# Optimization experiments

Hardware: AMD Instinct MI355X
Metric: run time of the kernel (lower is better)

Reference implementation:

```python
import jax, jax.numpy as jnp
import numpy as np

EPS_NORM = 1e-5   # RMSLayerNorm eps (hardcoded in __init__)
Q_EPS = 1e-5      # clamp floor for quantization scales (BitMat convention)


def _rmsnorm(x, w, eps):
    var = jnp.mean(jnp.square(x), axis=-1, keepdims=True)
    return x * jax.lax.rsqrt(var + eps) * w


def _weight_quant(w):
    # ternary (1.58-bit) quantization: scale = 1/mean(|W|), round+clip to {-1,0,1}
    scale = 1.0 / jnp.maximum(jnp.mean(jnp.abs(w)), Q_EPS)
    wq = jnp.clip(jnp.round(w * scale), -1.0, 1.0)
    return wq, scale


def _act_quant(x):
    # per-token int8 quantization: scale = 127/max(|x|) along last dim
    scale = 127.0 / jnp.maximum(jnp.max(jnp.abs(x), axis=-1, keepdims=True), Q_EPS)
    xq = jnp.clip(jnp.round(x * scale), -128.0, 127.0)
    return xq, scale


def setup_inputs() -> dict:
    key = jax.random.key(0)
    k1, k2 = jax.random.split(key)
    B, S, D = 4, 4096, 4096  # in_features == out_features == 4096
    x = jax.random.normal(k1, (B, S, D), dtype=jnp.float32)
    norm_weight = jnp.ones((D,), dtype=jnp.float32)
    # kaiming_normal fan_out relu: std = sqrt(2/out_features)
    weight = jax.random.normal(k2, (D, D), dtype=jnp.float32) * np.sqrt(2.0 / D)
    return {"x": x, "norm_weight": norm_weight, "weight": weight}


def reference(x, norm_weight, weight):
    h = _rmsnorm(x, norm_weight, EPS_NORM)            # [B,S,D]
    wq, sw = _weight_quant(weight)                    # [O,D], scalar
    hq, sx = _act_quant(h)                            # [B,S,D], [B,S,1]
    # integer-valued GEMM then dequant by both scales
    y = jnp.einsum('bsd,od->bso', hq, wq) / (sx * sw)
    return y
```

## Files before the change

kernel.cpp:

```cpp
#include <hip/hip_runtime.h>
#include <cstdint>
#include <cstddef>

typedef int v4i  __attribute__((ext_vector_type(4)));
typedef int v16i __attribute__((ext_vector_type(16)));

__device__ __forceinline__ void load_lds16(const void* g, void* l) {
    __builtin_amdgcn_global_load_lds(
        (const __attribute__((address_space(1))) void*)g,
        (__attribute__((address_space(3))) void*)l,
        16, 0, 0);
}

__global__ void wabs_sum_kernel(const float4* __restrict__ w4,
                                double* __restrict__ acc, int n4) {
    double s = 0.0;
    for (int i = blockIdx.x * blockDim.x + threadIdx.x; i < n4;
         i += gridDim.x * blockDim.x) {
        float4 v = w4[i];
        s += (double)fabsf(v.x) + (double)fabsf(v.y) +
             (double)fabsf(v.z) + (double)fabsf(v.w);
    }
    for (int o = 32; o > 0; o >>= 1) s += __shfl_down(s, o);
    __shared__ double sb[4];
    const int wid = threadIdx.x >> 6, lane = threadIdx.x & 63;
    if (lane == 0) sb[wid] = s;
    __syncthreads();
    if (threadIdx.x == 0) atomicAdd(acc, sb[0] + sb[1] + sb[2] + sb[3]);
}

__device__ __forceinline__ float sw_from_sum(const double* sump, int n) {
    float mean = (float)(*sump / (double)n);
    return 1.0f / fmaxf(mean, 1e-5f);
}

__global__ void wquant_kernel(const float4* __restrict__ w4,
                              const double* __restrict__ sump,
                              char4* __restrict__ wq4, int n4, int n) {
    const float s = sw_from_sum(sump, n);
    int i = blockIdx.x * blockDim.x + threadIdx.x;
    if (i >= n4) return;
    float4 v = w4[i];
    char4 q;
    q.x = (signed char)(int)fmaxf(-1.f, fminf(1.f, rintf(v.x * s)));
    q.y = (signed char)(int)fmaxf(-1.f, fminf(1.f, rintf(v.y * s)));
    q.z = (signed char)(int)fmaxf(-1.f, fminf(1.f, rintf(v.z * s)));
    q.w = (signed char)(int)fmaxf(-1.f, fminf(1.f, rintf(v.w * s)));
    wq4[i] = q;
}

__global__ __launch_bounds__(256) void act_quant_kernel(
    const float* __restrict__ x, const float* __restrict__ nw,
    const double* __restrict__ sump, int wcount,
    signed char* __restrict__ hq, float* __restrict__ rscale, int D) {
    const int m = blockIdx.x;
    const int t = threadIdx.x;
    const float4* xr  = (const float4*)(x + (size_t)m * D);
    const float4* nw4 = (const float4*)nw;

    float4 v[4];
    float ss = 0.f;
#pragma unroll
    for (int i = 0; i < 4; ++i) {
        v[i] = xr[t + 256 * i];
        ss += v[i].x * v[i].x + v[i].y * v[i].y +
              v[i].z * v[i].z + v[i].w * v[i].w;
    }
    for (int o = 32; o > 0; o >>= 1) ss += __shfl_down(ss, o);
    __shared__ float sb[4];
    const int wid = t >> 6, lane = t & 63;
    if (lane == 0) sb[wid] = ss;
    __syncthreads();
    const float var  = (sb[0] + sb[1] + sb[2] + sb[3]) / (float)D;
    const float rstd = (float)(1.0 / sqrt((double)var + 1e-5));
    __syncthreads();

    float mx = 0.f;
#pragma unroll
    for (int i = 0; i < 4; ++i) {
        float4 g = nw4[t + 256 * i];
        v[i].x = v[i].x * rstd * g.x;
        v[i].y = v[i].y * rstd * g.y;
        v[i].z = v[i].z * rstd * g.z;
        v[i].w = v[i].w * rstd * g.w;
        mx = fmaxf(mx, fmaxf(fmaxf(fabsf(v[i].x), fabsf(v[i].y)),
                             fmaxf(fabsf(v[i].z), fabsf(v[i].w))));
    }
    for (int o = 32; o > 0; o >>= 1) mx = fmaxf(mx, __shfl_down(mx, o));
    if (lane == 0) sb[wid] = mx;
    __syncthreads();
    const float mxa   = fmaxf(fmaxf(sb[0], sb[1]), fmaxf(sb[2], sb[3]));
    const float scale = 127.0f / fmaxf(mxa, 1e-5f);

    char4* hq4 = (char4*)(hq + (size_t)m * D);
#pragma unroll
    for (int i = 0; i < 4; ++i) {
        char4 q;
        q.x = (signed char)(int)fmaxf(-128.f, fminf(127.f, rintf(v[i].x * scale)));
        q.y = (signed char)(int)fmaxf(-128.f, fminf(127.f, rintf(v[i].y * scale)));
        q.z = (signed char)(int)fmaxf(-128.f, fminf(127.f, rintf(v[i].z * scale)));
        q.w = (signed char)(int)fmaxf(-128.f, fminf(127.f, rintf(v[i].w * scale)));
        hq4[t + 256 * i] = q;
    }
    if (t == 0) {
        const float sw = sw_from_sum(sump, wcount);
        rscale[m] = 1.0f / (scale * sw);
    }
}

__global__ __launch_bounds__(256) void gemm_i8_kernel(
    const signed char* __restrict__ A, const signed char* __restrict__ B,
    const float* __restrict__ rscale, float* __restrict__ out,
    int M, int N, int K) {
    constexpr int BM = 128, BN = 128, BK = 128;
    __shared__ signed char As[BM * BK];
    __shared__ signed char Bs[BN * BK];

    const int tid  = threadIdx.x;
    const int wave = tid >> 6;
    const int lane = tid & 63;
    const int wm   = wave >> 1;
    const int wn   = wave & 1;
    const int r32  = lane & 31;
    const int h    = lane >> 5;

    const int m0 = blockIdx.y * BM;
    const int n0 = blockIdx.x * BN;

    v16i acc[2][2] = {};

    const int srow = lane >> 3;
    const int skb  = ((lane & 7) ^ srow) * 16;
    const signed char* aSrc = A + (size_t)(m0 + wave * 32 + srow) * K + skb;
    const signed char* bSrc = B + (size_t)(n0 + wave * 32 + srow) * K + skb;

    for (int k0 = 0; k0 < K; k0 += BK) {
#pragma unroll
        for (int c = 0; c < 4; ++c) {
            load_lds16(aSrc + (size_t)(c * 8) * K + k0, &As[(wave * 4 + c) * 1024]);
            load_lds16(bSrc + (size_t)(c * 8) * K + k0, &Bs[(wave * 4 + c) * 1024]);
        }
        __syncthreads();

#pragma unroll
        for (int ks = 0; ks < 4; ++ks) {
            const int swz = ((ks * 2 + h) ^ (r32 & 7)) * 16;
            v4i af[2], bf[2];
#pragma unroll
            for (int mi = 0; mi < 2; ++mi)
                af[mi] = *(const v4i*)&As[(wm * 64 + mi * 32 + r32) * BK + swz];
#pragma unroll
            for (int ni = 0; ni < 2; ++ni)
                bf[ni] = *(const v4i*)&Bs[(wn * 64 + ni * 32 + r32) * BK + swz];
#pragma unroll
            for (int mi = 0; mi < 2; ++mi)
#pragma unroll
                for (int ni = 0; ni < 2; ++ni)
                    acc[mi][ni] = __builtin_amdgcn_mfma_i32_32x32x32_i8(
                        af[mi], bf[ni], acc[mi][ni], 0, 0, 0);
        }
        __syncthreads();
    }

#pragma unroll
    for (int mi = 0; mi < 2; ++mi) {
#pragma unroll
        for (int reg = 0; reg < 16; ++reg) {
            const int m = m0 + wm * 64 + mi * 32 + (reg & 3) + 8 * (reg >> 2) + 4 * h;
            const float rs = rscale[m];
            const size_t rowoff = (size_t)m * N + n0 + wn * 64 + r32;
#pragma unroll
            for (int ni = 0; ni < 2; ++ni)
                out[rowoff + ni * 32] = (float)acc[mi][ni][reg] * rs;
        }
    }
}

extern "C" void kernel_launch(void* const* d_in, const int* in_sizes, int n_in,
                              void* d_out, int out_size, void* d_ws, size_t ws_size,
                              hipStream_t stream) {
    const float* x  = (const float*)d_in[0];
    const float* nw = (const float*)d_in[1];
    const float* w  = (const float*)d_in[2];
    const int D = in_sizes[1];
    const int M = in_sizes[0] / D;
    const int O = in_sizes[2] / D;
    const int WN = O * D;

    char* ws = (char*)d_ws;
    double* d_sum    = (double*)(ws + 0);
    float*  d_rscale = (float*)(ws + 128);
    size_t off = 128 + (size_t)M * sizeof(float);
    off = (off + 255) & ~(size_t)255;
    signed char* d_wq = (signed char*)(ws + off);
    off += (size_t)WN;
    off = (off + 255) & ~(size_t)255;
    signed char* d_hq = (signed char*)(ws + off);

    hipMemsetAsync(d_sum, 0, sizeof(double), stream);

    wabs_sum_kernel<<<4096, 256, 0, stream>>>((const float4*)w, d_sum, WN / 4);

    wquant_kernel<<<(WN / 4 + 255) / 256, 256, 0, stream>>>(
        (const float4*)w, d_sum, (char4*)d_wq, WN / 4, WN);

    act_quant_kernel<<<M, 256, 0, stream>>>(x, nw, d_sum, WN, d_hq, d_rscale, D);

    dim3 grid(O / 128, M / 128);
    gemm_i8_kernel<<<grid, 256, 0, stream>>>(d_hq, d_wq, d_rscale,
                                             (float*)d_out, M, O, D);
}
```

Baseline: 800.0 us.

## Restructure int8 GEMM into 256x256 tiles with 4-stage LDS pipeline

The int8 MFMA GEMM grows from 128x128 tiles with 4 waves to 256x256 tiles with 8 waves, and BK drops to 64. Four LDS buffers are filled with async global-to-LDS loads three tiles ahead. Explicit vmcnt waits, raw barriers and s_setprio around the MFMA bursts overlap memory traffic with compute. Workgroup IDs are remapped so neighbouring blocks are spread across chiplets for better cache locality. The cost is 128KB of LDS per block, which limits occupancy to one block per CU, and a more fragile hand-managed pipeline.

```diff
diff --git a/kernel.cpp b/kernel.cpp
--- a/kernel.cpp
+++ b/kernel.cpp
@@ -108,70 +108,117 @@
     }
 }
 
-__global__ __launch_bounds__(256) void gemm_i8_kernel(
+constexpr int BM = 256, BN = 256, BK = 64;
+
+template<bool DO_STAGE, int VM>
+__device__ __forceinline__ void gemm_tile(
+    int t, signed char (*As)[BM * BK], signed char (*Bs)[BN * BK],
+    const signed char* aSrc, const signed char* bSrc, int K, int ldsOff,
+    int wm, int wn, int r32, int h, v16i (&acc)[4][2])
+{
+    const int buf = t & 3;
+    const int rb  = r32 & 3;
+#pragma unroll
+    for (int ks = 0; ks < 2; ++ks) {
+        v4i af[4], bf[2];
+        const int slot = ((2 * ks + h) ^ rb) * 16;
+#pragma unroll
+        for (int mf = 0; mf < 4; ++mf)
+            af[mf] = *(const v4i*)&As[buf][(wm * 128 + mf * 32 + r32) * BK + slot];
+#pragma unroll
+        for (int nf = 0; nf < 2; ++nf)
+            bf[nf] = *(const v4i*)&Bs[buf][(wn * 64 + nf * 32 + r32) * BK + slot];
+
+        if (DO_STAGE) {
+            const size_t kt = (size_t)(t + 3) * BK;
+            if (ks == 0) {
+                signed char* d = &As[(t + 3) & 3][ldsOff];
+                load_lds16(aSrc + kt, d);
+                load_lds16(aSrc + kt + (size_t)16 * K, d + 1024);
+            } else {
+                signed char* d = &Bs[(t + 3) & 3][ldsOff];
+                load_lds16(bSrc + kt, d);
+                load_lds16(bSrc + kt + (size_t)16 * K, d + 1024);
+            }
+        }
+        __builtin_amdgcn_s_barrier();
+        __builtin_amdgcn_s_setprio(1);
+#pragma unroll
+        for (int mf = 0; mf < 4; ++mf)
+#pragma unroll
+            for (int nf = 0; nf < 2; ++nf)
+                acc[mf][nf] = __builtin_amdgcn_mfma_i32_32x32x32_i8(
+                    af[mf], bf[nf], acc[mf][nf], 0, 0, 0);
+        __builtin_amdgcn_s_setprio(0);
+        if (ks == 1) {
+            if (VM == 8)      asm volatile("s_waitcnt vmcnt(8)" ::: "memory");
+            else if (VM == 4) asm volatile("s_waitcnt vmcnt(4)" ::: "memory");
+            else if (VM == 0) asm volatile("s_waitcnt vmcnt(0)" ::: "memory");
+        }
+        __builtin_amdgcn_s_barrier();
+    }
+}
+
+__global__ __launch_bounds__(512, 2) void gemm_i8_kernel(
     const signed char* __restrict__ A, const signed char* __restrict__ B,
     const float* __restrict__ rscale, float* __restrict__ out,
     int M, int N, int K) {
-    constexpr int BM = 128, BN = 128, BK = 128;
-    __shared__ signed char As[BM * BK];
-    __shared__ signed char Bs[BN * BK];
+    __shared__ signed char As[4][BM * BK];
+    __shared__ signed char Bs[4][BN * BK];
 
     const int tid  = threadIdx.x;
     const int wave = tid >> 6;
     const int lane = tid & 63;
-    const int wm   = wave >> 1;
-    const int wn   = wave & 1;
+    const int wm   = wave >> 2;
+    const int wn   = wave & 3;
     const int r32  = lane & 31;
     const int h    = lane >> 5;
 
-    const int m0 = blockIdx.y * BM;
-    const int n0 = blockIdx.x * BN;
-
-    v16i acc[2][2] = {};
-
-    const int srow = lane >> 3;
-    const int skb  = ((lane & 7) ^ srow) * 16;
-    const signed char* aSrc = A + (size_t)(m0 + wave * 32 + srow) * K + skb;
-    const signed char* bSrc = B + (size_t)(n0 + wave * 32 + srow) * K + skb;
-
-    for (int k0 = 0; k0 < K; k0 += BK) {
-#pragma unroll
-        for (int c = 0; c < 4; ++c) {
-            load_lds16(aSrc + (size_t)(c * 8) * K + k0, &As[(wave * 4 + c) * 1024]);
-            load_lds16(bSrc + (size_t)(c * 8) * K + k0, &Bs[(wave * 4 + c) * 1024]);
-        }
-        __syncthreads();
-
-#pragma unroll
-        for (int ks = 0; ks < 4; ++ks) {
-            const int swz = ((ks * 2 + h) ^ (r32 & 7)) * 16;
-            v4i af[2], bf[2];
-#pragma unroll
-            for (int mi = 0; mi < 2; ++mi)
-                af[mi] = *(const v4i*)&As[(wm * 64 + mi * 32 + r32) * BK + swz];
-#pragma unroll
-            for (int ni = 0; ni < 2; ++ni)
-                bf[ni] = *(const v4i*)&Bs[(wn * 64 + ni * 32 + r32) * BK + swz];
-#pragma unroll
-            for (int mi = 0; mi < 2; ++mi)
-#pragma unroll
-                for (int ni = 0; ni < 2; ++ni)
-                    acc[mi][ni] = __builtin_amdgcn_mfma_i32_32x32x32_i8(
-                        af[mi], bf[ni], acc[mi][ni], 0, 0, 0);
-        }
-        __syncthreads();
-    }
-
-#pragma unroll
-    for (int mi = 0; mi < 2; ++mi) {
+    const int nwg = gridDim.x * gridDim.y;
+    int lin = blockIdx.y * gridDim.x + blockIdx.x;
+    lin = (lin & 7) * (nwg >> 3) + (lin >> 3);
+    const int m0 = (lin / (int)gridDim.x) * BM;
+    const int n0 = (lin % (int)gridDim.x) * BN;
+
+    const int lrow = lane >> 2;
+    const int lswz = ((lane & 3) ^ (lrow & 3)) * 16;
+    const signed char* aSrc = A + (size_t)(m0 + wave * 32 + lrow) * K + lswz;
+    const signed char* bSrc = B + (size_t)(n0 + wave * 32 + lrow) * K + lswz;
+    const int ldsOff = wave * 2048;
+
+    v16i acc[4][2] = {};
+
+#pragma unroll
+    for (int p = 0; p < 3; ++p) {
+        const size_t kt = (size_t)p * BK;
+        signed char* da = &As[p][ldsOff];
+        signed char* db = &Bs[p][ldsOff];
+        load_lds16(aSrc + kt, da);
+        load_lds16(aSrc + kt + (size_t)16 * K, da + 1024);
+        load_lds16(bSrc + kt, db);
+        load_lds16(bSrc + kt + (size_t)16 * K, db + 1024);
+    }
+    asm volatile("s_waitcnt vmcnt(8)" ::: "memory");
+    __builtin_amdgcn_s_barrier();
+
+    const int NT = K >> 6;
+    int t = 0;
+    for (; t < NT - 3; ++t)
+        gemm_tile<true, 8>(t, As, Bs, aSrc, bSrc, K, ldsOff, wm, wn, r32, h, acc);
+    gemm_tile<false, 4>(NT - 3, As, Bs, aSrc, bSrc, K, ldsOff, wm, wn, r32, h, acc);
+    gemm_tile<false, 0>(NT - 2, As, Bs, aSrc, bSrc, K, ldsOff, wm, wn, r32, h, acc);
+    gemm_tile<false, -1>(NT - 1, As, Bs, aSrc, bSrc, K, ldsOff, wm, wn, r32, h, acc);
+
+#pragma unroll
+    for (int mf = 0; mf < 4; ++mf) {
 #pragma unroll
         for (int reg = 0; reg < 16; ++reg) {
-            const int m = m0 + wm * 64 + mi * 32 + (reg & 3) + 8 * (reg >> 2) + 4 * h;
+            const int m = m0 + wm * 128 + mf * 32 + (reg & 3) + 8 * (reg >> 2) + 4 * h;
             const float rs = rscale[m];
             const size_t rowoff = (size_t)m * N + n0 + wn * 64 + r32;
 #pragma unroll
-            for (int ni = 0; ni < 2; ++ni)
-                out[rowoff + ni * 32] = (float)acc[mi][ni][reg] * rs;
+            for (int nf = 0; nf < 2; ++nf)
+                out[rowoff + nf * 32] = (float)acc[mf][nf][reg] * rs;
         }
     }
 }
@@ -206,7 +253,7 @@
 
     act_quant_kernel<<<M, 256, 0, stream>>>(x, nw, d_sum, WN, d_hq, d_rscale, D);
 
-    dim3 grid(O / 128, M / 128);
-    gemm_i8_kernel<<<grid, 256, 0, stream>>>(d_hq, d_wq, d_rscale,
+    dim3 grid(O / 256, M / 256);
+    gemm_i8_kernel<<<grid, 512, 0, stream>>>(d_hq, d_wq, d_rscale,
                                              (float*)d_out, M, O, D);
 }
```

Measured after the change: 833.9 us. +4.2%, slower.
